# Kernel optimization log

Measured on AMD Instinct MI355X. Metric: run time of the kernel, lower is better.

Reference implementation:

```python
import jax, jax.numpy as jnp
import numpy as np

N_QUBITS = 14      # must be even (module assert)
IN_CHANNEL = 512   # batch of independent circuits

# PennyLane convention: wire 0 is the most-significant bit of the basis index.

def _mcx_perm(n, c1, c2, t):
    # MultiControlledX with control_values '10': flip target bit t when bit(c1)==1 and bit(c2)==0
    idx = np.arange(2 ** n)
    b1 = (idx >> (n - 1 - c1)) & 1
    b2 = (idx >> (n - 1 - c2)) & 1
    return np.where((b1 == 1) & (b2 == 0), idx ^ (1 << (n - 1 - t)), idx)

_MCX_PERMS = [jnp.asarray(_mcx_perm(N_QUBITS, w, (w + 1) % N_QUBITS, (w + 2) % N_QUBITS))
              for w in range(N_QUBITS)]
# Z-eigenvalue signs per basis state per wire: (2^n, n)
_Z_SIGNS = jnp.asarray(
    np.stack([1.0 - 2.0 * ((np.arange(2 ** N_QUBITS) >> (N_QUBITS - 1 - w)) & 1)
              for w in range(N_QUBITS)], axis=1), dtype=jnp.float32)


def _apply_rx(state, theta, w):
    # RX(theta) = [[cos(t/2), -i sin(t/2)], [-i sin(t/2), cos(t/2)]] on wire w; theta: (B,)
    B = state.shape[0]
    st = state.reshape(B, 2 ** w, 2, -1)
    c = jnp.cos(0.5 * theta)[:, None, None]
    s = (-1j * jnp.sin(0.5 * theta))[:, None, None]
    s0, s1 = st[:, :, 0, :], st[:, :, 1, :]
    out = jnp.stack([c * s0 + s * s1, c * s1 + s * s0], axis=2)
    return out.reshape(B, -1)


def _apply_rz(state, theta, w):
    # RZ(theta) = diag(e^{-i t/2}, e^{+i t/2}) on wire w
    B = state.shape[0]
    st = state.reshape(B, 2 ** w, 2, -1)
    p0 = jnp.exp(-0.5j * theta)[:, None, None]
    p1 = jnp.exp(0.5j * theta)[:, None, None]
    out = jnp.stack([p0 * st[:, :, 0, :], p1 * st[:, :, 1, :]], axis=2)
    return out.reshape(B, -1)


def _apply_isingxx(state, phi, wa, wb):
    a, b = min(wa, wb), max(wa, wb)
    B = state.shape[0]
    st = state.reshape(B, 2 ** a, 2, 2 ** (b - a - 1), 2, -1)
    c = jnp.cos(0.5 * phi)[:, None, None, None]
    s = (-1j * jnp.sin(0.5 * phi))[:, None, None, None]
    s00 = st[:, :, 0, :, 0, :]; s01 = st[:, :, 0, :, 1, :]
    s10 = st[:, :, 1, :, 0, :]; s11 = st[:, :, 1, :, 1, :]
    row0 = jnp.stack([c * s00 + s * s11, c * s01 + s * s10], axis=3)  # (B, 2^a, M, 2, R)
    row1 = jnp.stack([c * s10 + s * s01, c * s11 + s * s00], axis=3)
    return jnp.stack([row0, row1], axis=2).reshape(B, -1)


def _circuit(cp, p):
    n = N_QUBITS
    B = cp.shape[0]
    state = jnp.zeros((B, 2 ** n), dtype=jnp.complex64).at[:, 0].set(1.0)
    for w in range(n):
        state = _apply_rx(state, p[:, 0, w], w)
    for ws in range(n // 2):
        state = _apply_isingxx(state, cp[:, ws], 2 * ws, 2 * ws + 1)
    for w in range(n):
        state = _apply_rz(state, p[:, 1, w], w)
    for ws in range(n // 2):
        wss = 2 * ws + 1
        state = _apply_isingxx(state, cp[:, ws + n // 2], wss, (wss + 1) % n)
    for w in range(n):
        state = _apply_rx(state, p[:, 2, w], w)
    for w in range(n):
        state = state[:, _MCX_PERMS[w]]
    probs = state.real ** 2 + state.imag ** 2  # (B, 2^n)
    return (probs @ _Z_SIGNS).astype(jnp.float32)  # (B, n) = expval PauliZ per wire


def setup_inputs() -> dict:
    key = jax.random.key(0)
    k1, k2 = jax.random.split(key)
    cp = jax.random.uniform(k1, (IN_CHANNEL, N_QUBITS), dtype=jnp.float32) * jnp.pi
    p = jax.random.uniform(k2, (IN_CHANNEL, 3, N_QUBITS), dtype=jnp.float32) * jnp.pi
    return {"cp": cp, "p": p}


def reference(cp, p):
    return _circuit(cp, p)
```

## Files before the change

kernel.cpp:

```cpp
#include <hip/hip_runtime.h>

#define NQ 14
#define NSTATE (1 << NQ)
#define NT 256
#define AMPS 64

typedef float  f2  __attribute__((ext_vector_type(2)));
typedef __fp16 h2v __attribute__((ext_vector_type(2)));

#define N_H2 16640
#define OFF_BTAB  (N_H2*4)
#define OFF_RX3   (OFF_BTAB + 28*8)
#define OFF_XX2   (OFF_RX3 + 28*4)
#define OFF_RED   (OFF_XX2 + 14*4)
#define SMEM_BYTES (OFF_RED + 4*NQ*4)

__device__ __forceinline__ f2 cmul(f2 a, f2 b){
    f2 br = {-b.y, b.x};
    return a.x * b + a.y * br;
}

__device__ __forceinline__ f2 pkswz(f2 ss, f2 y){
    f2 t;
    asm("v_pk_mul_f32 %0, %1, %2 op_sel:[0,1] op_sel_hi:[1,0] neg_hi:[0,1]"
        : "=v"(t) : "v"(ss), "v"(y));
    return t;
}
__device__ __forceinline__ f2 pkfma(f2 a, f2 b, f2 c){
    f2 d;
    asm("v_pk_fma_f32 %0, %1, %2, %3" : "=v"(d) : "v"(a), "v"(b), "v"(c));
    return d;
}
__device__ __forceinline__ void rot2(f2& A, f2& B, f2 cc, f2 ss){
    f2 tA = pkswz(ss, B);
    f2 tB = pkswz(ss, A);
    A = pkfma(cc, A, tA);
    B = pkfma(cc, B, tB);
}

__device__ __forceinline__ h2v pack(f2 v){ return __builtin_amdgcn_cvt_pkrtz(v.x, v.y); }
__device__ __forceinline__ f2  unpack(h2v h){ return (f2){(float)h.x, (float)h.y}; }

template<int P, int M>
__device__ __forceinline__ void applyXX(f2* amp, f2 cc, f2 ss){
    #pragma unroll
    for (int L = 0; L < AMPS; ++L)
        if (!((L >> P) & 1)) rot2(amp[L], amp[L ^ M], cc, ss);
}
template<int R>
__device__ __forceinline__ void applyRX(f2* amp, f2 cc, f2 ss){
    #pragma unroll
    for (int L = 0; L < AMPS; ++L)
        if (!((L >> R) & 1)) rot2(amp[L], amp[L | (1 << R)], cc, ss);
}

__global__ void perm_tbl_kernel(unsigned short* __restrict__ tbl)
{
    const int j = blockIdx.x * blockDim.x + threadIdx.x;
    int x = j;
    #pragma unroll
    for (int w = 0; w < NQ; ++w) {
        const int p1 = 13 - w;
        const int p2 = 13 - ((w + 1) % NQ);
        const int pt = 13 - ((w + 2) % NQ);
        const int cond = ((x >> p1) & ~(x >> p2)) & 1;
        x ^= cond << pt;
    }
    const int t = ((j >> 1) & 15) | (((j >> 7) & 1) << 4) | (j & 0x60) | (((j >> 8) & 1) << 7);
    const int L = (j & 1) | (((j >> 13) & 1) << 1) | (((j >> 9) & 15) << 2);
    tbl[(L >> 3) * 2048 + t * 8 + (L & 7)] = (unsigned short)x;
}

__global__ void __launch_bounds__(NT, 2)
qsim_kernel(const float* __restrict__ cp, const float* __restrict__ p,
            const unsigned short* __restrict__ tblD, float* __restrict__ out)
{
    extern __shared__ __align__(16) char smem[];
    h2v* st    = reinterpret_cast<h2v*>(smem);
    f2*  Btab  = reinterpret_cast<f2*>(smem + OFF_BTAB);
    float* rx3c = reinterpret_cast<float*>(smem + OFF_RX3);
    float* rx3s = rx3c + 14;
    float* xx2c = reinterpret_cast<float*>(smem + OFF_XX2);
    float* xx2s = xx2c + 7;
    float* red  = reinterpret_cast<float*>(smem + OFF_RED);

    const int b = blockIdx.x;
    const int t = threadIdx.x;
    const float* pb  = p  + b * 42;
    const float* cpb = cp + b * 14;

    if (t < 7) {
        const int ws = t, wa = 2*ws, wb = 2*ws + 1;
        float sa, ca; sincosf(0.5f * pb[wa], &sa, &ca);
        float sb, cb; sincosf(0.5f * pb[wb], &sb, &cb);
        f2 s00 = {ca*cb, 0.f};
        f2 s01 = {0.f, -ca*sb};
        f2 s10 = {0.f, -sa*cb};
        f2 s11 = {-sa*sb, 0.f};
        float sx, cx; sincosf(0.5f * cpb[ws], &sx, &cx);
        rot2(s00, s11, (f2){cx,cx}, (f2){sx,sx});
        rot2(s01, s10, (f2){cx,cx}, (f2){sx,sx});
        const float ga = 0.5f * pb[14 + wa], gb = 0.5f * pb[14 + wb];
        float sA, cA; sincosf(ga + gb, &sA, &cA);
        float sB, cB; sincosf(gb - ga, &sB, &cB);
        s00 = cmul(s00, (f2){cA, -sA});
        s11 = cmul(s11, (f2){cA,  sA});
        s01 = cmul(s01, (f2){cB,  sB});
        s10 = cmul(s10, (f2){cB, -sB});
        const int k = 6 - ws;
        Btab[k*4+0] = s00; Btab[k*4+1] = s01; Btab[k*4+2] = s10; Btab[k*4+3] = s11;
    } else if (t >= 64 && t < 78) {
        const int w = t - 64;
        float s, c; sincosf(0.5f * pb[28 + w], &s, &c);
        rx3c[w] = c; rx3s[w] = s;
    } else if (t >= 128 && t < 135) {
        const int g = t - 128;
        float s, c; sincosf(0.5f * cpb[7 + g], &s, &c);
        xx2c[g] = c; xx2s[g] = s;
    }
    __syncthreads();

    f2 amp[AMPS];
    f2 cc, ss;
    #define LOADXX(g) do { float c_ = xx2c[g], s_ = xx2s[g]; cc = (f2){c_,c_}; ss = (f2){s_,s_}; } while (0)
    #define LOADRX(w) do { float c_ = rx3c[w], s_ = rx3s[w]; cc = (f2){c_,c_}; ss = (f2){s_,s_}; } while (0)


    {
        const int t6 = (t >> 6) & 1, t7 = t >> 7;
        f2 Pc = cmul(cmul(Btab[t & 3], Btab[4 + ((t >> 2) & 3)]), Btab[8 + ((t >> 4) & 3)]);
        f2 P3a0 = cmul(Pc, Btab[12 + t6]);
        f2 P3a1 = cmul(Pc, Btab[12 + 2 + t6]);
        f2 G00 = cmul(P3a0, Btab[24 + (t7 << 1)]);
        f2 G01 = cmul(P3a0, Btab[24 + (t7 << 1) + 1]);
        f2 G10 = cmul(P3a1, Btab[24 + (t7 << 1)]);
        f2 G11 = cmul(P3a1, Btab[24 + (t7 << 1) + 1]);
        #pragma unroll
        for (int m = 0; m < 16; ++m) {
            f2 H = cmul(Btab[16 + (m & 3)], Btab[20 + (m >> 2)]);
            amp[(m << 1)]          = cmul(G00, H);
            amp[(m << 1) | 1]      = cmul(G10, H);
            amp[32 | (m << 1)]     = cmul(G01, H);
            amp[32 | (m << 1) | 1] = cmul(G11, H);
        }
        LOADXX(0); applyXX<5, 0x30>(amp, cc, ss);
        LOADXX(1); applyXX<3, 0x0C>(amp, cc, ss);
        LOADXX(2); applyXX<1, 0x03>(amp, cc, ss);
        LOADRX(1); applyRX<5>(amp, cc, ss);
        LOADRX(2); applyRX<4>(amp, cc, ss);
        LOADRX(3); applyRX<3>(amp, cc, ss);
        LOADRX(4); applyRX<2>(amp, cc, ss);
        LOADRX(5); applyRX<1>(amp, cc, ss);
        LOADRX(6); applyRX<0>(amp, cc, ss);
        const int jbase = (t7 << 13) | (t & 127);
        #pragma unroll
        for (int L = 0; L < AMPS; ++L) {
            const int j = jbase | (L << 7);
            st[j ^ ((j >> 7) & 127)] = pack(amp[L]);
        }
    }
    __syncthreads();

    {
        const int t0 = t & 1, thi = t >> 1;
        const int hi7 = thi << 7;
        #pragma unroll
        for (int L = 0; L < AMPS; ++L)
            amp[L] = unpack(st[hi7 | (((L << 1) | t0) ^ thi)]);
        LOADXX(3); applyXX<5, 0x30>(amp, cc, ss);
        LOADXX(4); applyXX<3, 0x0C>(amp, cc, ss);
        LOADXX(5); applyXX<1, 0x03>(amp, cc, ss);
        LOADRX(7);  applyRX<5>(amp, cc, ss);
        LOADRX(8);  applyRX<4>(amp, cc, ss);
        LOADRX(9);  applyRX<3>(amp, cc, ss);
        LOADRX(10); applyRX<2>(amp, cc, ss);
        LOADRX(11); applyRX<1>(amp, cc, ss);
        LOADRX(12); applyRX<0>(amp, cc, ss);
        #pragma unroll
        for (int L = 0; L < AMPS; ++L)
            st[hi7 | (((L << 1) | t0) ^ thi)] = pack(amp[L]);
    }
    __syncthreads();

    {
        uint4 tv[8];
        const uint4* tq = reinterpret_cast<const uint4*>(tblD);
        #pragma unroll
        for (int g = 0; g < 8; ++g) tv[g] = tq[g * 256 + t];

        const int tbase = ((t & 15) << 1) | (t & 0x60) | (((t >> 4) & 1) << 7) | (((t >> 7) & 1) << 8);
        #pragma unroll
        for (int L = 0; L < AMPS; ++L) {
            const int j = tbase | (L & 1) | (((L >> 1) & 1) << 13) | (((L >> 2) & 15) << 9);
            amp[L] = unpack(st[j ^ ((j >> 7) & 127)]);
        }
        LOADXX(6);  applyXX<0, 0x03>(amp, cc, ss);
        LOADRX(13); applyRX<0>(amp, cc, ss);
        LOADRX(0);  applyRX<1>(amp, cc, ss);
        __syncthreads();
        #pragma unroll
        for (int L = 0; L < AMPS; ++L) {
            const unsigned comp = (L & 4) ? ((L & 2) ? tv[L >> 3].w : tv[L >> 3].z)
                                          : ((L & 2) ? tv[L >> 3].y : tv[L >> 3].x);
            const unsigned f = (L & 1) ? (comp >> 16) : (comp & 0xffffu);
            st[f + (f >> 6)] = pack(amp[L]);
        }
    }
    __syncthreads();

    {
        const h2v* erow = st + t * 65;
        float U0, U1 = 0.f, U2 = 0.f, U4, U5, T;
        float C[8];
        float u0acc = 0.f;
        #pragma unroll
        for (int ch = 0; ch < 8; ++ch) {
            float q[8];
            #pragma unroll
            for (int e = 0; e < 8; ++e) {
                const f2 a = unpack(erow[ch * 8 + e]);
                q[e] = fmaf(a.x, a.x, a.y * a.y);
            }
            const float p0 = q[0] + q[1], p1 = q[2] + q[3], p2 = q[4] + q[5], p3 = q[6] + q[7];
            u0acc += (q[1] + q[3]) + (q[5] + q[7]);
            U1 += p1 + p3;
            const float s01 = p0 + p1, s23 = p2 + p3;
            U2 += s23;
            C[ch] = s01 + s23;
        }
        U0 = u0acc;
        {
            const float P0 = C[0] + C[1], P1 = C[2] + C[3], P2 = C[4] + C[5], P3v = C[6] + C[7];
            const float U3v = (C[1] + C[3]) + (C[5] + C[7]);
            U4 = P1 + P3v;
            const float Q0 = P0 + P1, Q1 = P2 + P3v;
            U5 = Q1;
            T = Q0 + Q1;
            U2 += 0.f;
            C[0] = U3v;
        }
        const float U3 = C[0];

        float s = T;
        float d0, d1, d2, d3, d4, d5;
        {
            float o;
            o = __shfl_xor(s, 1);  d0 = s - o; s += o;
            o = __shfl_xor(d0, 2); d0 += o;
            o = __shfl_xor(s, 2);  d1 = s - o; s += o;
            o = __shfl_xor(d0, 4); d0 += o;
            o = __shfl_xor(d1, 4); d1 += o;
            o = __shfl_xor(s, 4);  d2 = s - o; s += o;
            o = __shfl_xor(d0, 8); d0 += o;
            o = __shfl_xor(d1, 8); d1 += o;
            o = __shfl_xor(d2, 8); d2 += o;
            o = __shfl_xor(s, 8);  d3 = s - o; s += o;
            o = __shfl_xor(d0, 16); d0 += o;
            o = __shfl_xor(d1, 16); d1 += o;
            o = __shfl_xor(d2, 16); d2 += o;
            o = __shfl_xor(d3, 16); d3 += o;
            o = __shfl_xor(s, 16);  d4 = s - o; s += o;
            o = __shfl_xor(d0, 32); d0 += o;
            o = __shfl_xor(d1, 32); d1 += o;
            o = __shfl_xor(d2, 32); d2 += o;
            o = __shfl_xor(d3, 32); d3 += o;
            o = __shfl_xor(d4, 32); d4 += o;
            o = __shfl_xor(s, 32);  d5 = s - o; s += o;
        }
        float V0 = U0, V1 = U1, V2 = U2, V3 = U3, V4 = U4, V5 = U5;
        #pragma unroll
        for (int m = 1; m < 64; m <<= 1) {
            V0 += __shfl_xor(V0, m);
            V1 += __shfl_xor(V1, m);
            V2 += __shfl_xor(V2, m);
            V3 += __shfl_xor(V3, m);
            V4 += __shfl_xor(V4, m);
            V5 += __shfl_xor(V5, m);
        }
        if ((t & 63) == 0) {
            const int wv = t >> 6;
            float* r = red + wv * NQ;
            r[0]  = (wv & 2) ? -s : s;
            r[1]  = (wv & 1) ? -s : s;
            r[2]  = d5;
            r[3]  = d4;
            r[4]  = d3;
            r[5]  = d2;
            r[6]  = d1;
            r[7]  = d0;
            r[8]  = s - 2.f * V5;
            r[9]  = s - 2.f * V4;
            r[10] = s - 2.f * V3;
            r[11] = s - 2.f * V2;
            r[12] = s - 2.f * V1;
            r[13] = s - 2.f * V0;
        }
    }
    __syncthreads();
    if (t < NQ) {
        out[b * NQ + t] = (red[t] + red[NQ + t]) + (red[2 * NQ + t] + red[3 * NQ + t]);
    }
    #undef LOADXX
    #undef LOADRX
}

extern "C" void kernel_launch(void* const* d_in, const int* in_sizes, int n_in,
                              void* d_out, int out_size, void* d_ws, size_t ws_size,
                              hipStream_t stream)
{
    (void)n_in; (void)out_size; (void)ws_size;
    const float* cp = (const float*)d_in[0];
    const float* p  = (const float*)d_in[1];
    float* out = (float*)d_out;
    unsigned short* tbl = (unsigned short*)d_ws;
    const int B = in_sizes[0] / NQ;

    perm_tbl_kernel<<<NSTATE / 256, 256, 0, stream>>>(tbl);

    (void)hipFuncSetAttribute(reinterpret_cast<const void*>(qsim_kernel),
                              hipFuncAttributeMaxDynamicSharedMemorySize, SMEM_BYTES);
    qsim_kernel<<<B, NT, SMEM_BYTES, stream>>>(cp, p, tbl, out);
}
```

Measured before the change: 79.35 us.

## Merge last two gate stages using DPP cross-lane exchanges for wires 13/0

Redistributes amplitudes so that the final XX(13,0), RX(13) and RX(0) gates act on bits held across lanes within a quad. They are applied with DPP quad permutes instead of a separate shared-memory exchange. This removes one full LDS store/load round trip and a barrier, and changes the swizzle and permutation table layout to match. In exchange it adds two DPP moves per amplitude per gate and relies on the new lane mapping being correct.

```diff
diff --git a/kernel.cpp b/kernel.cpp
--- a/kernel.cpp
+++ b/kernel.cpp
@@ -40,6 +40,13 @@
 
 __device__ __forceinline__ h2v pack(f2 v){ return __builtin_amdgcn_cvt_pkrtz(v.x, v.y); }
 __device__ __forceinline__ f2  unpack(h2v h){ return (f2){(float)h.x, (float)h.y}; }
+
+template<int CTRL>
+__device__ __forceinline__ f2 qperm(f2 v){
+    int x = __builtin_amdgcn_mov_dpp(__float_as_int(v.x), CTRL, 0xf, 0xf, true);
+    int y = __builtin_amdgcn_mov_dpp(__float_as_int(v.y), CTRL, 0xf, 0xf, true);
+    return (f2){__int_as_float(x), __int_as_float(y)};
+}
 
 template<int P, int M>
 __device__ __forceinline__ void applyXX(f2* amp, f2 cc, f2 ss){
@@ -66,8 +73,11 @@
         const int cond = ((x >> p1) & ~(x >> p2)) & 1;
         x ^= cond << pt;
     }
-    const int t = ((j >> 1) & 15) | (((j >> 7) & 1) << 4) | (j & 0x60) | (((j >> 8) & 1) << 7);
-    const int L = (j & 1) | (((j >> 13) & 1) << 1) | (((j >> 9) & 15) << 2);
+    const int L  = (j >> 1) & 63;
+    const int l  = (j & 1) | (((j >> 13) & 1) << 1) | (((j >> 12) & 1) << 2)
+                 | (((j >> 11) & 1) << 3) | (((j >> 10) & 1) << 4) | (((j >> 9) & 1) << 5);
+    const int w_ = (((j >> 7) & 1) << 1) | ((j >> 8) & 1);
+    const int t  = (w_ << 6) | l;
     tbl[(L >> 3) * 2048 + t * 8 + (L & 7)] = (unsigned short)x;
 }
 
@@ -125,7 +135,6 @@
     #define LOADXX(g) do { float c_ = xx2c[g], s_ = xx2s[g]; cc = (f2){c_,c_}; ss = (f2){s_,s_}; } while (0)
     #define LOADRX(w) do { float c_ = rx3c[w], s_ = rx3s[w]; cc = (f2){c_,c_}; ss = (f2){s_,s_}; } while (0)
 
-
     {
         const int t6 = (t >> 6) & 1, t7 = t >> 7;
         f2 Pc = cmul(cmul(Btab[t & 3], Btab[4 + ((t >> 2) & 3)]), Btab[8 + ((t >> 4) & 3)]);
@@ -152,21 +161,30 @@
         LOADRX(4); applyRX<2>(amp, cc, ss);
         LOADRX(5); applyRX<1>(amp, cc, ss);
         LOADRX(6); applyRX<0>(amp, cc, ss);
-        const int jbase = (t7 << 13) | (t & 127);
+        const int jhi = (t7 << 13) | (t & 127);
         #pragma unroll
         for (int L = 0; L < AMPS; ++L) {
-            const int j = jbase | (L << 7);
-            st[j ^ ((j >> 7) & 127)] = pack(amp[L]);
+            const int j = jhi | (L << 7);
+            st[j ^ ((j >> 9) & 31)] = pack(amp[L]);
         }
     }
     __syncthreads();
 
     {
-        const int t0 = t & 1, thi = t >> 1;
-        const int hi7 = thi << 7;
+        uint4 tv[8];
+        const uint4* tq = reinterpret_cast<const uint4*>(tblD);
+        #pragma unroll
+        for (int g = 0; g < 8; ++g) tv[g] = tq[g * 256 + t];
+
+        const int l = t & 63, w_ = t >> 6;
+        const int jbase = (l & 1) | (((w_ >> 1) & 1) << 7) | ((w_ & 1) << 8)
+                        | (((l >> 5) & 1) << 9) | (((l >> 4) & 1) << 10)
+                        | (((l >> 3) & 1) << 11) | (((l >> 2) & 1) << 12)
+                        | (((l >> 1) & 1) << 13);
+        const int jb2 = jbase ^ ((jbase >> 9) & 31);
         #pragma unroll
         for (int L = 0; L < AMPS; ++L)
-            amp[L] = unpack(st[hi7 | (((L << 1) | t0) ^ thi)]);
+            amp[L] = unpack(st[jb2 ^ (L << 1)]);
         LOADXX(3); applyXX<5, 0x30>(amp, cc, ss);
         LOADXX(4); applyXX<3, 0x0C>(amp, cc, ss);
         LOADXX(5); applyXX<1, 0x03>(amp, cc, ss);
@@ -176,27 +194,15 @@
         LOADRX(10); applyRX<2>(amp, cc, ss);
         LOADRX(11); applyRX<1>(amp, cc, ss);
         LOADRX(12); applyRX<0>(amp, cc, ss);
-        #pragma unroll
-        for (int L = 0; L < AMPS; ++L)
-            st[hi7 | (((L << 1) | t0) ^ thi)] = pack(amp[L]);
-    }
-    __syncthreads();
-
-    {
-        uint4 tv[8];
-        const uint4* tq = reinterpret_cast<const uint4*>(tblD);
-        #pragma unroll
-        for (int g = 0; g < 8; ++g) tv[g] = tq[g * 256 + t];
-
-        const int tbase = ((t & 15) << 1) | (t & 0x60) | (((t >> 4) & 1) << 7) | (((t >> 7) & 1) << 8);
-        #pragma unroll
-        for (int L = 0; L < AMPS; ++L) {
-            const int j = tbase | (L & 1) | (((L >> 1) & 1) << 13) | (((L >> 2) & 15) << 9);
-            amp[L] = unpack(st[j ^ ((j >> 7) & 127)]);
-        }
-        LOADXX(6);  applyXX<0, 0x03>(amp, cc, ss);
-        LOADRX(13); applyRX<0>(amp, cc, ss);
-        LOADRX(0);  applyRX<1>(amp, cc, ss);
+        LOADXX(6);
+        #pragma unroll
+        for (int L = 0; L < AMPS; ++L) { f2 pv = qperm<0x1B>(amp[L]); amp[L] = pkfma(cc, amp[L], pkswz(ss, pv)); }
+        LOADRX(13);
+        #pragma unroll
+        for (int L = 0; L < AMPS; ++L) { f2 pv = qperm<0xB1>(amp[L]); amp[L] = pkfma(cc, amp[L], pkswz(ss, pv)); }
+        LOADRX(0);
+        #pragma unroll
+        for (int L = 0; L < AMPS; ++L) { f2 pv = qperm<0x4E>(amp[L]); amp[L] = pkfma(cc, amp[L], pkswz(ss, pv)); }
         __syncthreads();
         #pragma unroll
         for (int L = 0; L < AMPS; ++L) {
@@ -236,7 +242,6 @@
             const float Q0 = P0 + P1, Q1 = P2 + P3v;
             U5 = Q1;
             T = Q0 + Q1;
-            U2 += 0.f;
             C[0] = U3v;
         }
         const float U3 = C[0];
```

Result: no change. 80.16 us (+1.0%).

## Split state across 512 threads with 32 amplitudes each and DPP cross-lane gates

Applied to the files above, without the earlier changes.

Doubles the threads per block to 512 and halves the amplitudes per thread to 32, then redesigns every stage around the new split. This covers the shared-memory swizzles and stage decomposition, the permutation table layout, and the final reduction across 8 wavefronts. Gates on the lowest qubit bit, now spread across adjacent lanes, are applied with DPP quad permutes instead of going through shared memory. The aim is lower register pressure and higher occupancy, at the cost of more cross-lane work and a larger reduction.

```diff
diff --git a/kernel.cpp b/kernel.cpp
--- a/kernel.cpp
+++ b/kernel.cpp
@@ -2,8 +2,8 @@
 
 #define NQ 14
 #define NSTATE (1 << NQ)
-#define NT 256
-#define AMPS 64
+#define NT 512
+#define AMPS 32
 
 typedef float  f2  __attribute__((ext_vector_type(2)));
 typedef __fp16 h2v __attribute__((ext_vector_type(2)));
@@ -13,7 +13,7 @@
 #define OFF_RX3   (OFF_BTAB + 28*8)
 #define OFF_XX2   (OFF_RX3 + 28*4)
 #define OFF_RED   (OFF_XX2 + 14*4)
-#define SMEM_BYTES (OFF_RED + 4*NQ*4)
+#define SMEM_BYTES (OFF_RED + 8*NQ*4)
 
 __device__ __forceinline__ f2 cmul(f2 a, f2 b){
     f2 br = {-b.y, b.x};
@@ -40,6 +40,13 @@
 
 __device__ __forceinline__ h2v pack(f2 v){ return __builtin_amdgcn_cvt_pkrtz(v.x, v.y); }
 __device__ __forceinline__ f2  unpack(h2v h){ return (f2){(float)h.x, (float)h.y}; }
+
+template<int CTRL>
+__device__ __forceinline__ f2 qperm(f2 v){
+    int x = __builtin_amdgcn_mov_dpp(__float_as_int(v.x), CTRL, 0xf, 0xf, true);
+    int y = __builtin_amdgcn_mov_dpp(__float_as_int(v.y), CTRL, 0xf, 0xf, true);
+    return (f2){__int_as_float(x), __int_as_float(y)};
+}
 
 template<int P, int M>
 __device__ __forceinline__ void applyXX(f2* amp, f2 cc, f2 ss){
@@ -66,12 +73,12 @@
         const int cond = ((x >> p1) & ~(x >> p2)) & 1;
         x ^= cond << pt;
     }
-    const int t = ((j >> 1) & 15) | (((j >> 7) & 1) << 4) | (j & 0x60) | (((j >> 8) & 1) << 7);
-    const int L = (j & 1) | (((j >> 13) & 1) << 1) | (((j >> 9) & 15) << 2);
-    tbl[(L >> 3) * 2048 + t * 8 + (L & 7)] = (unsigned short)x;
-}
-
-__global__ void __launch_bounds__(NT, 2)
+    const int L = j & 31;
+    const int t = (j >> 13) | (((j >> 5) & 0xFF) << 1);
+    tbl[t * 32 + L] = (unsigned short)x;
+}
+
+__global__ void __launch_bounds__(NT, 4)
 qsim_kernel(const float* __restrict__ cp, const float* __restrict__ p,
             const unsigned short* __restrict__ tblD, float* __restrict__ out)
 {
@@ -125,78 +132,88 @@
     #define LOADXX(g) do { float c_ = xx2c[g], s_ = xx2s[g]; cc = (f2){c_,c_}; ss = (f2){s_,s_}; } while (0)
     #define LOADRX(w) do { float c_ = rx3c[w], s_ = rx3s[w]; cc = (f2){c_,c_}; ss = (f2){s_,s_}; } while (0)
 
-
     {
-        const int t6 = (t >> 6) & 1, t7 = t >> 7;
-        f2 Pc = cmul(cmul(Btab[t & 3], Btab[4 + ((t >> 2) & 3)]), Btab[8 + ((t >> 4) & 3)]);
-        f2 P3a0 = cmul(Pc, Btab[12 + t6]);
-        f2 P3a1 = cmul(Pc, Btab[12 + 2 + t6]);
-        f2 G00 = cmul(P3a0, Btab[24 + (t7 << 1)]);
-        f2 G01 = cmul(P3a0, Btab[24 + (t7 << 1) + 1]);
-        f2 G10 = cmul(P3a1, Btab[24 + (t7 << 1)]);
-        f2 G11 = cmul(P3a1, Btab[24 + (t7 << 1) + 1]);
-        #pragma unroll
-        for (int m = 0; m < 16; ++m) {
-            f2 H = cmul(Btab[16 + (m & 3)], Btab[20 + (m >> 2)]);
-            amp[(m << 1)]          = cmul(G00, H);
-            amp[(m << 1) | 1]      = cmul(G10, H);
-            amp[32 | (m << 1)]     = cmul(G01, H);
-            amp[32 | (m << 1) | 1] = cmul(G11, H);
-        }
-        LOADXX(0); applyXX<5, 0x30>(amp, cc, ss);
-        LOADXX(1); applyXX<3, 0x0C>(amp, cc, ss);
-        LOADXX(2); applyXX<1, 0x03>(amp, cc, ss);
-        LOADRX(1); applyRX<5>(amp, cc, ss);
-        LOADRX(2); applyRX<4>(amp, cc, ss);
-        LOADRX(3); applyRX<3>(amp, cc, ss);
-        LOADRX(4); applyRX<2>(amp, cc, ss);
-        LOADRX(5); applyRX<1>(amp, cc, ss);
-        LOADRX(6); applyRX<0>(amp, cc, ss);
-        const int jbase = (t7 << 13) | (t & 127);
-        #pragma unroll
-        for (int L = 0; L < AMPS; ++L) {
-            const int j = jbase | (L << 7);
-            st[j ^ ((j >> 7) & 127)] = pack(amp[L]);
+        const int t8 = t >> 8;
+        f2 Pc = cmul(cmul(Btab[t & 3], Btab[4 + ((t >> 2) & 3)]),
+                     cmul(Btab[8 + ((t >> 4) & 3)], Btab[12 + ((t >> 6) & 3)]));
+        f2 G0 = cmul(Pc, Btab[24 + (t8 << 1)]);
+        f2 G1 = cmul(Pc, Btab[24 + (t8 << 1) + 1]);
+        f2 H[16];
+        #pragma unroll
+        for (int m = 0; m < 16; ++m)
+            H[m] = cmul(Btab[16 + (m & 3)], Btab[20 + (m >> 2)]);
+        #pragma unroll
+        for (int L = 0; L < AMPS; ++L)
+            amp[L] = cmul((L & 16) ? G1 : G0, H[L & 15]);
+        LOADXX(0); applyXX<4, 0x18>(amp, cc, ss);
+        LOADXX(1); applyXX<2, 0x06>(amp, cc, ss);
+        LOADRX(1); applyRX<4>(amp, cc, ss);
+        LOADRX(2); applyRX<3>(amp, cc, ss);
+        LOADRX(3); applyRX<2>(amp, cc, ss);
+        LOADRX(4); applyRX<1>(amp, cc, ss);
+        LOADRX(5); applyRX<0>(amp, cc, ss);
+        const int jhi = ((t >> 8) << 13) | (t & 255);
+        #pragma unroll
+        for (int L = 0; L < AMPS; ++L) {
+            const int j = jhi | (L << 8);
+            st[j ^ ((j >> 5) & 31)] = pack(amp[L]);
         }
     }
     __syncthreads();
 
     {
-        const int t0 = t & 1, thi = t >> 1;
-        const int hi7 = thi << 7;
+        const int jb = (t & 15) | (((t >> 4) & 15) << 9) | ((t >> 8) << 13);
+        #pragma unroll
+        for (int L = 0; L < AMPS; ++L) {
+            const int j = jb | (L << 4);
+            amp[L] = unpack(st[j ^ ((j >> 5) & 31)]);
+        }
+        LOADXX(2); applyXX<4, 0x18>(amp, cc, ss);
+        LOADXX(3); applyXX<2, 0x06>(amp, cc, ss);
+        LOADRX(6); applyRX<3>(amp, cc, ss);
+        LOADRX(7); applyRX<2>(amp, cc, ss);
+        LOADRX(8); applyRX<1>(amp, cc, ss);
+        LOADRX(9); applyRX<0>(amp, cc, ss);
+        #pragma unroll
+        for (int L = 0; L < AMPS; ++L) {
+            const int j = jb | (L << 4);
+            st[j ^ ((j >> 5) & 31)] = pack(amp[L]);
+        }
+    }
+    __syncthreads();
+
+    {
+        uint4 tv[4];
+        {
+            const uint4* tq = reinterpret_cast<const uint4*>(tblD) + t * 4;
+            #pragma unroll
+            for (int g = 0; g < 4; ++g) tv[g] = tq[g];
+        }
+        const int jb3 = ((t & 1) << 13) | ((t >> 1) << 5);
+        const int xr  = (jb3 >> 5) & 31;
         #pragma unroll
         for (int L = 0; L < AMPS; ++L)
-            amp[L] = unpack(st[hi7 | (((L << 1) | t0) ^ thi)]);
-        LOADXX(3); applyXX<5, 0x30>(amp, cc, ss);
-        LOADXX(4); applyXX<3, 0x0C>(amp, cc, ss);
-        LOADXX(5); applyXX<1, 0x03>(amp, cc, ss);
-        LOADRX(7);  applyRX<5>(amp, cc, ss);
-        LOADRX(8);  applyRX<4>(amp, cc, ss);
-        LOADRX(9);  applyRX<3>(amp, cc, ss);
-        LOADRX(10); applyRX<2>(amp, cc, ss);
-        LOADRX(11); applyRX<1>(amp, cc, ss);
-        LOADRX(12); applyRX<0>(amp, cc, ss);
-        #pragma unroll
-        for (int L = 0; L < AMPS; ++L)
-            st[hi7 | (((L << 1) | t0) ^ thi)] = pack(amp[L]);
-    }
-    __syncthreads();
-
-    {
-        uint4 tv[8];
-        const uint4* tq = reinterpret_cast<const uint4*>(tblD);
-        #pragma unroll
-        for (int g = 0; g < 8; ++g) tv[g] = tq[g * 256 + t];
-
-        const int tbase = ((t & 15) << 1) | (t & 0x60) | (((t >> 4) & 1) << 7) | (((t >> 7) & 1) << 8);
-        #pragma unroll
-        for (int L = 0; L < AMPS; ++L) {
-            const int j = tbase | (L & 1) | (((L >> 1) & 1) << 13) | (((L >> 2) & 15) << 9);
-            amp[L] = unpack(st[j ^ ((j >> 7) & 127)]);
-        }
-        LOADXX(6);  applyXX<0, 0x03>(amp, cc, ss);
+            amp[L] = unpack(st[jb3 + (L ^ xr)]);
+        LOADXX(4); applyXX<4, 0x18>(amp, cc, ss);
+        LOADXX(5); applyXX<2, 0x06>(amp, cc, ss);
+        LOADRX(10); applyRX<3>(amp, cc, ss);
+        LOADRX(11); applyRX<2>(amp, cc, ss);
+        LOADRX(12); applyRX<1>(amp, cc, ss);
         LOADRX(13); applyRX<0>(amp, cc, ss);
-        LOADRX(0);  applyRX<1>(amp, cc, ss);
+        LOADXX(6);
+        #pragma unroll
+        for (int L = 0; L < AMPS; L += 2) {
+            f2 pv0 = qperm<0xB1>(amp[L + 1]);
+            f2 pv1 = qperm<0xB1>(amp[L]);
+            amp[L]     = pkfma(cc, amp[L],     pkswz(ss, pv0));
+            amp[L + 1] = pkfma(cc, amp[L + 1], pkswz(ss, pv1));
+        }
+        LOADRX(0);
+        #pragma unroll
+        for (int L = 0; L < AMPS; ++L) {
+            f2 pv = qperm<0xB1>(amp[L]);
+            amp[L] = pkfma(cc, amp[L], pkswz(ss, pv));
+        }
         __syncthreads();
         #pragma unroll
         for (int L = 0; L < AMPS; ++L) {
@@ -209,12 +226,11 @@
     __syncthreads();
 
     {
-        const h2v* erow = st + t * 65;
-        float U0, U1 = 0.f, U2 = 0.f, U4, U5, T;
-        float C[8];
-        float u0acc = 0.f;
-        #pragma unroll
-        for (int ch = 0; ch < 8; ++ch) {
+        const h2v* erow = st + t * 32 + (t >> 1);
+        float U0 = 0.f, U1 = 0.f, U2 = 0.f;
+        float C[4];
+        #pragma unroll
+        for (int ch = 0; ch < 4; ++ch) {
             float q[8];
             #pragma unroll
             for (int e = 0; e < 8; ++e) {
@@ -222,24 +238,15 @@
                 q[e] = fmaf(a.x, a.x, a.y * a.y);
             }
             const float p0 = q[0] + q[1], p1 = q[2] + q[3], p2 = q[4] + q[5], p3 = q[6] + q[7];
-            u0acc += (q[1] + q[3]) + (q[5] + q[7]);
+            U0 += (q[1] + q[3]) + (q[5] + q[7]);
             U1 += p1 + p3;
             const float s01 = p0 + p1, s23 = p2 + p3;
             U2 += s23;
             C[ch] = s01 + s23;
         }
-        U0 = u0acc;
-        {
-            const float P0 = C[0] + C[1], P1 = C[2] + C[3], P2 = C[4] + C[5], P3v = C[6] + C[7];
-            const float U3v = (C[1] + C[3]) + (C[5] + C[7]);
-            U4 = P1 + P3v;
-            const float Q0 = P0 + P1, Q1 = P2 + P3v;
-            U5 = Q1;
-            T = Q0 + Q1;
-            U2 += 0.f;
-            C[0] = U3v;
-        }
-        const float U3 = C[0];
+        const float U3 = C[1] + C[3];
+        const float U4 = C[2] + C[3];
+        const float T  = (C[0] + C[1]) + (C[2] + C[3]);
 
         float s = T;
         float d0, d1, d2, d3, d4, d5;
@@ -267,7 +274,7 @@
             o = __shfl_xor(d4, 32); d4 += o;
             o = __shfl_xor(s, 32);  d5 = s - o; s += o;
         }
-        float V0 = U0, V1 = U1, V2 = U2, V3 = U3, V4 = U4, V5 = U5;
+        float V0 = U0, V1 = U1, V2 = U2, V3 = U3, V4 = U4;
         #pragma unroll
         for (int m = 1; m < 64; m <<= 1) {
             V0 += __shfl_xor(V0, m);
@@ -275,20 +282,19 @@
             V2 += __shfl_xor(V2, m);
             V3 += __shfl_xor(V3, m);
             V4 += __shfl_xor(V4, m);
-            V5 += __shfl_xor(V5, m);
         }
         if ((t & 63) == 0) {
             const int wv = t >> 6;
             float* r = red + wv * NQ;
-            r[0]  = (wv & 2) ? -s : s;
-            r[1]  = (wv & 1) ? -s : s;
-            r[2]  = d5;
-            r[3]  = d4;
-            r[4]  = d3;
-            r[5]  = d2;
-            r[6]  = d1;
-            r[7]  = d0;
-            r[8]  = s - 2.f * V5;
+            r[0]  = (wv & 4) ? -s : s;
+            r[1]  = (wv & 2) ? -s : s;
+            r[2]  = (wv & 1) ? -s : s;
+            r[3]  = d5;
+            r[4]  = d4;
+            r[5]  = d3;
+            r[6]  = d2;
+            r[7]  = d1;
+            r[8]  = d0;
             r[9]  = s - 2.f * V4;
             r[10] = s - 2.f * V3;
             r[11] = s - 2.f * V2;
@@ -298,7 +304,10 @@
     }
     __syncthreads();
     if (t < NQ) {
-        out[b * NQ + t] = (red[t] + red[NQ + t]) + (red[2 * NQ + t] + red[3 * NQ + t]);
+        float ssum = 0.f;
+        #pragma unroll
+        for (int wv = 0; wv < 8; ++wv) ssum += red[wv * NQ + t];
+        out[b * NQ + t] = ssum;
     }
     #undef LOADXX
     #undef LOADRX
```

New measurement: 79.15 us. About the same (-0.3%).
